# Kernel tuning notes

Measured on AMD Instinct MI355X. Metric: run time of the kernel, lower is better.

Reference implementation:

```python
import jax, jax.numpy as jnp
import numpy as np

EMBED_DIM = 1024
NUM_HEADS = 16
HEAD_DIM = 64
B, S = 4, 2048


def setup_inputs() -> dict:
    key = jax.random.key(0)
    ks = jax.random.split(key, 5)
    std = 0.02
    x = jax.random.normal(ks[0], (B, S, EMBED_DIM), dtype=jnp.float32)
    Wq = std * jax.random.normal(ks[1], (NUM_HEADS, EMBED_DIM, HEAD_DIM), dtype=jnp.float32)
    Wk = std * jax.random.normal(ks[2], (NUM_HEADS, EMBED_DIM, HEAD_DIM), dtype=jnp.float32)
    Wv = std * jax.random.normal(ks[3], (NUM_HEADS, EMBED_DIM, HEAD_DIM), dtype=jnp.float32)
    Wo = std * jax.random.normal(ks[4], (NUM_HEADS, HEAD_DIM, EMBED_DIM), dtype=jnp.float32)
    bq = jnp.zeros((NUM_HEADS, HEAD_DIM), dtype=jnp.float32)
    bk = jnp.zeros((NUM_HEADS, HEAD_DIM), dtype=jnp.float32)
    bv = jnp.zeros((NUM_HEADS, HEAD_DIM), dtype=jnp.float32)
    bo = jnp.zeros((EMBED_DIM,), dtype=jnp.float32)
    return {"x": x, "Wq": Wq, "bq": bq, "Wk": Wk, "bk": bk,
            "Wv": Wv, "bv": bv, "Wo": Wo, "bo": bo}


def reference(x, Wq, bq, Wk, bk, Wv, bv, Wo, bo):
    # q,k,v: [b, s, n, h]
    q = jnp.einsum('bsd,ndh->bsnh', x, Wq) + bq
    k = jnp.einsum('bsd,ndh->bsnh', x, Wk) + bk
    v = jnp.einsum('bsd,ndh->bsnh', x, Wv) + bv
    scale = 1.0 / (HEAD_DIM ** 0.5)
    # non-causal full attention matrix [b, n, s, t]
    attn = jnp.einsum('bsnh,btnh->bnst', q, k) * scale
    attn = jax.nn.softmax(attn, axis=-1)
    after = jnp.einsum('bnst,btnh->bsnh', attn, v)
    out = jnp.einsum('bsnh,nhd->bsd', after, Wo) + bo
    return out
```

## Files before the change

### kernel.cpp

```cpp
#include <hip/hip_runtime.h>

typedef __bf16 bf16;
typedef bf16 bf16x8 __attribute__((ext_vector_type(8)));
typedef bf16 bf16x4 __attribute__((ext_vector_type(4)));
typedef float f32x4 __attribute__((ext_vector_type(4)));

constexpr int Bb = 4, Ss = 2048, Dd = 1024, NH = 16, HD = 64;
constexpr int BS = Bb * Ss;
constexpr int QKV_LD = 3 * Dd;
constexpr float CSC = 0.18033688011112042f;

__device__ __forceinline__ int sw(int row, int col) {
  return (row << 6) + (col ^ ((row & 7) << 3));
}

__device__ __forceinline__ void g2l16(const bf16* g, bf16* l) {
  __builtin_amdgcn_global_load_lds(
      (const __attribute__((address_space(1))) void*)g,
      (__attribute__((address_space(3))) void*)l, 16, 0, 0);
}

__global__ void convert_x(const float* __restrict__ x, bf16* __restrict__ xb) {
  int o = (blockIdx.x * 256 + threadIdx.x) * 4;
  f32x4 v = *(const f32x4*)&x[o];
  bf16x4 r = {(bf16)v[0], (bf16)v[1], (bf16)v[2], (bf16)v[3]};
  *(bf16x4*)&xb[o] = r;
}

__global__ void prep_weights(const float* __restrict__ Wq, const float* __restrict__ Wk,
                             const float* __restrict__ Wv, const float* __restrict__ Wo,
                             const float* __restrict__ bq, const float* __restrict__ bk,
                             const float* __restrict__ bv,
                             bf16* __restrict__ WT_all, bf16* __restrict__ WoT,
                             float* __restrict__ bias_all) {
  int o = blockIdx.x * 256 + threadIdx.x;
  int sel = blockIdx.y;
  if (sel < 3) {
    const float* W = (sel == 0) ? Wq : (sel == 1) ? Wk : Wv;
    float scale = (sel == 0) ? CSC : 1.0f;
    int nq = o >> 10, d = o & 1023;
    int head = nq >> 6, h = nq & 63;
    WT_all[(sel << 20) + o] = (bf16)(W[head * 65536 + d * 64 + h] * scale);
    if (o < 1024) {
      const float* bb = (sel == 0) ? bq : (sel == 1) ? bk : bv;
      bias_all[sel * 1024 + o] = bb[o] * scale;
    }
  } else {
    int dd = o >> 10, c = o & 1023;
    WoT[o] = (bf16)Wo[c * 1024 + dd];
  }
}

template <typename OutT, bool VOUT>
__global__ __launch_bounds__(256) void gemm128(const bf16* __restrict__ A,
                                               const bf16* __restrict__ BT,
                                               const float* __restrict__ bias,
                                               OutT* __restrict__ C, int ldc,
                                               bf16* __restrict__ VTout) {
  __shared__ __align__(16) bf16 As[128 * 64];
  __shared__ __align__(16) bf16 Bs[128 * 64];
  const int t = threadIdx.x;
  const int w = t >> 6, l = t & 63, q = l >> 4, lm = l & 15;
  const int wm = w & 1, wn = w >> 1;
  const int m0 = blockIdx.x * 128, n0 = blockIdx.y * 128;
  constexpr int K = 1024;
  int ro[4], co[4];
#pragma unroll
  for (int i = 0; i < 4; ++i) {
    int o = i * 256 + t;
    ro[i] = o >> 3;
    co[i] = ((o & 7) ^ ((o >> 3) & 7)) << 3;
  }
  const int lbase = (t & 192) * 8;
  f32x4 acc[4][4] = {};
  for (int k0 = 0; k0 < K; k0 += 64) {
    __syncthreads();
#pragma unroll
    for (int i = 0; i < 4; ++i)
      g2l16(&A[(size_t)(m0 + ro[i]) * K + k0 + co[i]], &As[i * 2048 + lbase]);
#pragma unroll
    for (int i = 0; i < 4; ++i)
      g2l16(&BT[(size_t)(n0 + ro[i]) * K + k0 + co[i]], &Bs[i * 2048 + lbase]);
    __syncthreads();
#pragma unroll
    for (int kh = 0; kh < 2; ++kh) {
      bf16x8 a[4], b[4];
#pragma unroll
      for (int i = 0; i < 4; ++i)
        a[i] = *(const bf16x8*)&As[sw(wm * 64 + i * 16 + lm, kh * 32 + q * 8)];
#pragma unroll
      for (int i = 0; i < 4; ++i)
        b[i] = *(const bf16x8*)&Bs[sw(wn * 64 + i * 16 + lm, kh * 32 + q * 8)];
#pragma unroll
      for (int mt = 0; mt < 4; ++mt)
#pragma unroll
        for (int nt = 0; nt < 4; ++nt)
          acc[mt][nt] = __builtin_amdgcn_mfma_f32_16x16x32_bf16(a[mt], b[nt], acc[mt][nt], 0, 0, 0);
    }
  }
  if (VOUT && n0 >= 2048) {
#pragma unroll
    for (int nt = 0; nt < 4; ++nt) {
      int colg = n0 + wn * 64 + nt * 16 + lm;
      float bb = bias[colg];
      int bnh = colg - 2048;
      size_t vbase = (size_t)(bnh >> 6) * 131072 + (size_t)(bnh & 63) * 2048;
#pragma unroll
      for (int mt = 0; mt < 4; ++mt) {
        int row = m0 + wm * 64 + mt * 16 + q * 4;
#pragma unroll
        for (int r = 0; r < 4; ++r) {
          int m = row + r;
          VTout[(size_t)((m >> 11) << 4) * 131072 + vbase + (m & 2047)] =
              (bf16)(acc[mt][nt][r] + bb);
        }
      }
    }
  } else {
#pragma unroll
    for (int nt = 0; nt < 4; ++nt) {
      int col = n0 + wn * 64 + nt * 16 + lm;
      float bb = bias[col];
#pragma unroll
      for (int mt = 0; mt < 4; ++mt) {
        int row = m0 + wm * 64 + mt * 16 + q * 4;
#pragma unroll
        for (int r = 0; r < 4; ++r)
          C[(size_t)(row + r) * ldc + col] = (OutT)(acc[mt][nt][r] + bb);
      }
    }
  }
}

__global__ __launch_bounds__(256) void attn(const bf16* __restrict__ QKV,
                                            const bf16* __restrict__ VT,
                                            bf16* __restrict__ after) {
  __shared__ __align__(16) bf16 QPs[128 * 64];
  __shared__ __align__(16) bf16 Ks[2][64 * 64];
  __shared__ __align__(16) bf16 Vs[2][64 * 64];
  const int t = threadIdx.x;
  const int w = t >> 6, l = t & 63, q = l >> 4, lm = l & 15;
  const int s0 = blockIdx.x * 128;
  const int bn = blockIdx.y, b = bn >> 4, n = bn & 15;
  const bf16* Qb = QKV + (size_t)(b * 2048) * QKV_LD + n * 64;
  const bf16* Kb = Qb + 1024;
  const bf16* Vtb = VT + (size_t)bn * 64 * 2048;
  int ro[4], co[4];
#pragma unroll
  for (int i = 0; i < 4; ++i) {
    int o = i * 256 + t;
    ro[i] = o >> 3;
    co[i] = ((o & 7) ^ ((o >> 3) & 7)) << 3;
  }
  const int lbase = (t & 192) * 8;
#pragma unroll
  for (int i = 0; i < 4; ++i)
    g2l16(&Qb[(size_t)(s0 + ro[i]) * QKV_LD + co[i]], &QPs[i * 2048 + lbase]);
  __syncthreads();
  bf16x8 qa[2][2];
#pragma unroll
  for (int mt = 0; mt < 2; ++mt)
#pragma unroll
    for (int kh = 0; kh < 2; ++kh)
      qa[mt][kh] = *(const bf16x8*)&QPs[sw(w * 32 + mt * 16 + lm, kh * 32 + q * 8)];

  f32x4 o_acc[2][4] = {};
  float rs[2] = {0.f, 0.f};
  for (int t0 = 0; t0 < Ss; t0 += 128) {
    __syncthreads();
#pragma unroll
    for (int j = 0; j < 2; ++j)
#pragma unroll
      for (int i = 0; i < 2; ++i) {
        g2l16(&Kb[(size_t)(t0 + j * 64 + ro[i]) * QKV_LD + co[i]], &Ks[j][i * 2048 + lbase]);
        g2l16(&Vtb[(size_t)ro[i] * 2048 + t0 + j * 64 + co[i]], &Vs[j][i * 2048 + lbase]);
      }
    __syncthreads();
#pragma unroll
    for (int j = 0; j < 2; ++j) {
      f32x4 sc[2][4] = {};
#pragma unroll
      for (int kh = 0; kh < 2; ++kh) {
        bf16x8 kb[4];
#pragma unroll
        for (int c = 0; c < 4; ++c)
          kb[c] = *(const bf16x8*)&Ks[j][sw(c * 16 + lm, kh * 32 + q * 8)];
#pragma unroll
        for (int mt = 0; mt < 2; ++mt)
#pragma unroll
          for (int c = 0; c < 4; ++c)
            sc[mt][c] = __builtin_amdgcn_mfma_f32_16x16x32_bf16(kb[c], qa[mt][kh], sc[mt][c], 0, 0, 0);
      }
#pragma unroll
      for (int mt = 0; mt < 2; ++mt) {
        int s = w * 32 + mt * 16 + lm;
#pragma unroll
        for (int c = 0; c < 4; ++c) {
          bf16x4 pk;
#pragma unroll
          for (int r = 0; r < 4; ++r) {
            float p = __builtin_amdgcn_exp2f(sc[mt][c][r]);
            rs[mt] += p;
            pk[r] = (bf16)p;
          }
          *(bf16x4*)&QPs[(s << 6) + ((((c << 2) + q) ^ lm) << 2)] = pk;
        }
      }
#pragma unroll
      for (int kh = 0; kh < 2; ++kh) {
        bf16x8 pa[2], vb[4];
#pragma unroll
        for (int mt = 0; mt < 2; ++mt) {
          int s = w * 32 + mt * 16 + lm;
          bf16x4 lo = *(const bf16x4*)&QPs[(s << 6) + ((((kh << 3) + (q << 1)) ^ lm) << 2)];
          bf16x4 hi = *(const bf16x4*)&QPs[(s << 6) + ((((kh << 3) + (q << 1) + 1) ^ lm) << 2)];
          pa[mt] = __builtin_shufflevector(lo, hi, 0, 1, 2, 3, 4, 5, 6, 7);
        }
#pragma unroll
        for (int c = 0; c < 4; ++c)
          vb[c] = *(const bf16x8*)&Vs[j][sw(c * 16 + lm, kh * 32 + q * 8)];
#pragma unroll
        for (int mt = 0; mt < 2; ++mt)
#pragma unroll
          for (int c = 0; c < 4; ++c)
            o_acc[mt][c] = __builtin_amdgcn_mfma_f32_16x16x32_bf16(pa[mt], vb[c], o_acc[mt][c], 0, 0, 0);
      }
    }
  }
#pragma unroll
  for (int mt = 0; mt < 2; ++mt) {
    float v = rs[mt];
    v += __shfl_xor(v, 16);
    v += __shfl_xor(v, 32);
    rs[mt] = v;
  }
#pragma unroll
  for (int mt = 0; mt < 2; ++mt)
#pragma unroll
    for (int r = 0; r < 4; ++r) {
      float inv = 1.f / __shfl(rs[mt], q * 4 + r);
      int srow = s0 + w * 32 + mt * 16 + q * 4 + r;
      size_t base = (size_t)(b * 2048 + srow) * 1024 + n * 64;
#pragma unroll
      for (int c = 0; c < 4; ++c)
        after[base + c * 16 + lm] = (bf16)(o_acc[mt][c][r] * inv);
    }
}

extern "C" void kernel_launch(void* const* d_in, const int* in_sizes, int n_in,
                              void* d_out, int out_size, void* d_ws, size_t ws_size,
                              hipStream_t stream) {
  const float* x  = (const float*)d_in[0];
  const float* Wq = (const float*)d_in[1];
  const float* bq = (const float*)d_in[2];
  const float* Wk = (const float*)d_in[3];
  const float* bk = (const float*)d_in[4];
  const float* Wv = (const float*)d_in[5];
  const float* bv = (const float*)d_in[6];
  const float* Wo = (const float*)d_in[7];
  const float* bo = (const float*)d_in[8];
  float* out = (float*)d_out;

  bf16* WT_all    = (bf16*)d_ws;
  bf16* WoT       = WT_all + (size_t)3072 * 1024;
  float* bias_all = (float*)(WoT + (size_t)1024 * 1024);
  bf16* xb        = (bf16*)(bias_all + 4096);
  bf16* QKVb      = xb + (size_t)BS * Dd;
  bf16* VTb       = QKVb + (size_t)BS * QKV_LD;
  bf16* after     = VTb + (size_t)Bb * NH * HD * Ss;

  convert_x<<<dim3(BS * Dd / 1024), dim3(256), 0, stream>>>(x, xb);
  prep_weights<<<dim3(4096, 4), dim3(256), 0, stream>>>(Wq, Wk, Wv, Wo, bq, bk, bv,
                                                        WT_all, WoT, bias_all);
  gemm128<bf16, true><<<dim3(BS / 128, 24), dim3(256), 0, stream>>>(xb, WT_all, bias_all,
                                                                    QKVb, QKV_LD, VTb);
  attn<<<dim3(Ss / 128, Bb * NH), dim3(256), 0, stream>>>(QKVb, VTb, after);
  gemm128<float, false><<<dim3(BS / 128, 8), dim3(256), 0, stream>>>(after, WoT, bo,
                                                                     out, 1024, nullptr);
}
```

Before: 300.9 us.

## Tile weight transposes, split V projection into transposed GEMM, double-buffer attention loads

Weight preparation now transposes through shared-memory tiles with vectorized loads and stores instead of strided scalar gathers. The V projection runs as a separate GEMM with swapped operands, so the transposed V layout is written directly. The attention kernel now software-pipelines K/V tiles: the next 64-key tile is prefetched into a double buffer while the current one is computed, and it uses one barrier per iteration. Row sums are computed with an MFMA against a ones vector instead of scalar adds and shuffles, the P buffer gets a padded layout, occupancy is hinted at 3 blocks, and blocks are remapped for L2 locality. This adds one kernel launch and makes the synchronization more intricate.

```diff
diff --git a/kernel.cpp b/kernel.cpp
--- a/kernel.cpp
+++ b/kernel.cpp
@@ -7,7 +7,6 @@
 
 constexpr int Bb = 4, Ss = 2048, Dd = 1024, NH = 16, HD = 64;
 constexpr int BS = Bb * Ss;
-constexpr int QKV_LD = 3 * Dd;
 constexpr float CSC = 0.18033688011112042f;
 
 __device__ __forceinline__ int sw(int row, int col) {
@@ -27,41 +26,74 @@
   *(bf16x4*)&xb[o] = r;
 }
 
-__global__ void prep_weights(const float* __restrict__ Wq, const float* __restrict__ Wk,
-                             const float* __restrict__ Wv, const float* __restrict__ Wo,
-                             const float* __restrict__ bq, const float* __restrict__ bk,
-                             const float* __restrict__ bv,
-                             bf16* __restrict__ WT_all, bf16* __restrict__ WoT,
-                             float* __restrict__ bias_all) {
-  int o = blockIdx.x * 256 + threadIdx.x;
-  int sel = blockIdx.y;
+__global__ void prep(const float* __restrict__ Wq, const float* __restrict__ Wk,
+                     const float* __restrict__ Wv, const float* __restrict__ Wo,
+                     const float* __restrict__ bq, const float* __restrict__ bk,
+                     const float* __restrict__ bv,
+                     bf16* __restrict__ WT_all, bf16* __restrict__ WoT,
+                     float* __restrict__ bias_all) {
+  __shared__ bf16 Ts[64 * 72];
+  const int t = threadIdx.x;
+  const int sel = blockIdx.y;
   if (sel < 3) {
     const float* W = (sel == 0) ? Wq : (sel == 1) ? Wk : Wv;
     float scale = (sel == 0) ? CSC : 1.0f;
-    int nq = o >> 10, d = o & 1023;
-    int head = nq >> 6, h = nq & 63;
-    WT_all[(sel << 20) + o] = (bf16)(W[head * 65536 + d * 64 + h] * scale);
-    if (o < 1024) {
-      const float* bb = (sel == 0) ? bq : (sel == 1) ? bk : bv;
-      bias_all[sel * 1024 + o] = bb[o] * scale;
-    }
-  } else {
-    int dd = o >> 10, c = o & 1023;
-    WoT[o] = (bf16)Wo[c * 1024 + dd];
-  }
-}
-
-template <typename OutT, bool VOUT>
+    int head = blockIdx.x >> 4, dt = blockIdx.x & 15;
+    const float* src = W + head * 65536 + dt * 64 * 64;
+#pragma unroll
+    for (int i = 0; i < 4; ++i) {
+      int idx = i * 256 + t;
+      int dr = idx >> 4, hc = (idx & 15) * 4;
+      f32x4 v = *(const f32x4*)&src[dr * 64 + hc];
+#pragma unroll
+      for (int k = 0; k < 4; ++k) Ts[(hc + k) * 72 + dr] = (bf16)(v[k] * scale);
+    }
+    __syncthreads();
+    bf16* dst = WT_all + (size_t)sel * 1048576 + (size_t)(head * 64) * 1024 + dt * 64;
+#pragma unroll
+    for (int i = 0; i < 2; ++i) {
+      int idx = i * 256 + t;
+      int hr = idx >> 3, ch = (idx & 7) * 8;
+      *(bf16x8*)&dst[(size_t)hr * 1024 + ch] = *(const bf16x8*)&Ts[hr * 72 + ch];
+    }
+  } else if (sel == 3) {
+    int ct = blockIdx.x >> 4, dt = blockIdx.x & 15;
+    const float* src = Wo + (size_t)(ct * 64) * 1024 + dt * 64;
+#pragma unroll
+    for (int i = 0; i < 4; ++i) {
+      int idx = i * 256 + t;
+      int cr = idx >> 4, dc = (idx & 15) * 4;
+      f32x4 v = *(const f32x4*)&src[(size_t)cr * 1024 + dc];
+#pragma unroll
+      for (int k = 0; k < 4; ++k) Ts[(dc + k) * 72 + cr] = (bf16)v[k];
+    }
+    __syncthreads();
+    bf16* dst = WoT + (size_t)(dt * 64) * 1024 + ct * 64;
+#pragma unroll
+    for (int i = 0; i < 2; ++i) {
+      int idx = i * 256 + t;
+      int dr = idx >> 3, ch = (idx & 7) * 8;
+      *(bf16x8*)&dst[(size_t)dr * 1024 + ch] = *(const bf16x8*)&Ts[dr * 72 + ch];
+    }
+  } else if (blockIdx.x == 0) {
+    for (int j = t; j < 3072; j += 256) {
+      int s2 = j >> 10;
+      const float* bb = (s2 == 0) ? bq : (s2 == 1) ? bk : bv;
+      bias_all[j] = bb[j & 1023] * (s2 == 0 ? CSC : 1.0f);
+    }
+  }
+}
+
+template <int EPI>
 __global__ __launch_bounds__(256) void gemm128(const bf16* __restrict__ A,
                                                const bf16* __restrict__ BT,
                                                const float* __restrict__ bias,
-                                               OutT* __restrict__ C, int ldc,
-                                               bf16* __restrict__ VTout) {
+                                               void* __restrict__ Cv, int ldc) {
   __shared__ __align__(16) bf16 As[128 * 64];
   __shared__ __align__(16) bf16 Bs[128 * 64];
   const int t = threadIdx.x;
-  const int w = t >> 6, l = t & 63, q = l >> 4, lm = l & 15;
-  const int wm = w & 1, wn = w >> 1;
+  const int l = t & 63, q = l >> 4, lm = l & 15;
+  const int w = t >> 6, wm = w & 1, wn = w >> 1;
   const int m0 = blockIdx.x * 128, n0 = blockIdx.y * 128;
   constexpr int K = 1024;
   int ro[4], co[4];
@@ -98,23 +130,20 @@
           acc[mt][nt] = __builtin_amdgcn_mfma_f32_16x16x32_bf16(a[mt], b[nt], acc[mt][nt], 0, 0, 0);
     }
   }
-  if (VOUT && n0 >= 2048) {
+  if (EPI == 1) {
+    bf16* VT = (bf16*)Cv;
 #pragma unroll
     for (int nt = 0; nt < 4; ++nt) {
-      int colg = n0 + wn * 64 + nt * 16 + lm;
-      float bb = bias[colg];
-      int bnh = colg - 2048;
-      size_t vbase = (size_t)(bnh >> 6) * 131072 + (size_t)(bnh & 63) * 2048;
-#pragma unroll
-      for (int mt = 0; mt < 4; ++mt) {
-        int row = m0 + wm * 64 + mt * 16 + q * 4;
+      int sg = n0 + wn * 64 + nt * 16 + lm;
+      size_t sb = (size_t)(sg >> 11) * 2097152 + (sg & 2047);
+#pragma unroll
+      for (int mt = 0; mt < 4; ++mt)
 #pragma unroll
         for (int r = 0; r < 4; ++r) {
-          int m = row + r;
-          VTout[(size_t)((m >> 11) << 4) * 131072 + vbase + (m & 2047)] =
-              (bf16)(acc[mt][nt][r] + bb);
+          int m = m0 + wm * 64 + mt * 16 + q * 4 + r;
+          VT[sb + (size_t)(m >> 6) * 131072 + (size_t)(m & 63) * 2048] =
+              (bf16)(acc[mt][nt][r] + bias[m]);
         }
-      }
     }
   } else {
 #pragma unroll
@@ -125,26 +154,32 @@
       for (int mt = 0; mt < 4; ++mt) {
         int row = m0 + wm * 64 + mt * 16 + q * 4;
 #pragma unroll
-        for (int r = 0; r < 4; ++r)
-          C[(size_t)(row + r) * ldc + col] = (OutT)(acc[mt][nt][r] + bb);
+        for (int r = 0; r < 4; ++r) {
+          if (EPI == 2)
+            ((float*)Cv)[(size_t)(row + r) * ldc + col] = acc[mt][nt][r] + bb;
+          else
+            ((bf16*)Cv)[(size_t)(row + r) * ldc + col] = (bf16)(acc[mt][nt][r] + bb);
+        }
       }
     }
   }
 }
 
-__global__ __launch_bounds__(256) void attn(const bf16* __restrict__ QKV,
-                                            const bf16* __restrict__ VT,
-                                            bf16* __restrict__ after) {
-  __shared__ __align__(16) bf16 QPs[128 * 64];
+__global__ __launch_bounds__(256, 3) void attn(const bf16* __restrict__ QK,
+                                               const bf16* __restrict__ VT,
+                                               bf16* __restrict__ after) {
   __shared__ __align__(16) bf16 Ks[2][64 * 64];
   __shared__ __align__(16) bf16 Vs[2][64 * 64];
+  __shared__ __align__(16) bf16 Ps[128 * 72];
   const int t = threadIdx.x;
-  const int w = t >> 6, l = t & 63, q = l >> 4, lm = l & 15;
-  const int s0 = blockIdx.x * 128;
-  const int bn = blockIdx.y, b = bn >> 4, n = bn & 15;
-  const bf16* Qb = QKV + (size_t)(b * 2048) * QKV_LD + n * 64;
+  const int l = t & 63, q = l >> 4, lm = l & 15, w = t >> 6;
+  const int f = blockIdx.x;
+  const int bn = (f & 7) | ((f >> 7) << 3);
+  const int s0 = ((f >> 3) & 15) * 128;
+  const int b = bn >> 4, n = bn & 15;
+  const bf16* Qb = QK + (size_t)(b * 2048) * 2048 + n * 64;
   const bf16* Kb = Qb + 1024;
-  const bf16* Vtb = VT + (size_t)bn * 64 * 2048;
+  const bf16* Vtb = VT + (size_t)bn * 131072;
   int ro[4], co[4];
 #pragma unroll
   for (int i = 0; i < 4; ++i) {
@@ -153,92 +188,87 @@
     co[i] = ((o & 7) ^ ((o >> 3) & 7)) << 3;
   }
   const int lbase = (t & 192) * 8;
+  bf16* Kflat = &Ks[0][0];
 #pragma unroll
   for (int i = 0; i < 4; ++i)
-    g2l16(&Qb[(size_t)(s0 + ro[i]) * QKV_LD + co[i]], &QPs[i * 2048 + lbase]);
+    g2l16(&Qb[(size_t)(s0 + ro[i]) * 2048 + co[i]], Kflat + i * 2048 + lbase);
   __syncthreads();
   bf16x8 qa[2][2];
 #pragma unroll
   for (int mt = 0; mt < 2; ++mt)
 #pragma unroll
     for (int kh = 0; kh < 2; ++kh)
-      qa[mt][kh] = *(const bf16x8*)&QPs[sw(w * 32 + mt * 16 + lm, kh * 32 + q * 8)];
-
+      qa[mt][kh] = *(const bf16x8*)&Kflat[sw(w * 32 + mt * 16 + lm, kh * 32 + q * 8)];
+  __syncthreads();
+#pragma unroll
+  for (int i = 0; i < 2; ++i) {
+    g2l16(&Kb[(size_t)ro[i] * 2048 + co[i]], &Ks[0][i * 2048 + lbase]);
+    g2l16(&Vtb[(size_t)ro[i] * 2048 + co[i]], &Vs[0][i * 2048 + lbase]);
+  }
   f32x4 o_acc[2][4] = {};
-  float rs[2] = {0.f, 0.f};
-  for (int t0 = 0; t0 < Ss; t0 += 128) {
-    __syncthreads();
-#pragma unroll
-    for (int j = 0; j < 2; ++j)
+  f32x4 rsum[2] = {};
+  const bf16x8 ones = {(bf16)1.f, (bf16)1.f, (bf16)1.f, (bf16)1.f,
+                       (bf16)1.f, (bf16)1.f, (bf16)1.f, (bf16)1.f};
+  for (int rd = 0; rd < 32; ++rd) {
+    const int cur = rd & 1;
+    __syncthreads();
+    if (rd < 31) {
+      int t0n = (rd + 1) * 64, nb = cur ^ 1;
 #pragma unroll
       for (int i = 0; i < 2; ++i) {
-        g2l16(&Kb[(size_t)(t0 + j * 64 + ro[i]) * QKV_LD + co[i]], &Ks[j][i * 2048 + lbase]);
-        g2l16(&Vtb[(size_t)ro[i] * 2048 + t0 + j * 64 + co[i]], &Vs[j][i * 2048 + lbase]);
+        g2l16(&Kb[(size_t)(t0n + ro[i]) * 2048 + co[i]], &Ks[nb][i * 2048 + lbase]);
+        g2l16(&Vtb[(size_t)ro[i] * 2048 + t0n + co[i]], &Vs[nb][i * 2048 + lbase]);
       }
-    __syncthreads();
-#pragma unroll
-    for (int j = 0; j < 2; ++j) {
-      f32x4 sc[2][4] = {};
-#pragma unroll
-      for (int kh = 0; kh < 2; ++kh) {
-        bf16x8 kb[4];
+    }
+    f32x4 sc[2][4] = {};
+#pragma unroll
+    for (int kh = 0; kh < 2; ++kh) {
+      bf16x8 kb[4];
+#pragma unroll
+      for (int c = 0; c < 4; ++c)
+        kb[c] = *(const bf16x8*)&Ks[cur][sw(c * 16 + lm, kh * 32 + q * 8)];
+#pragma unroll
+      for (int mt = 0; mt < 2; ++mt)
 #pragma unroll
         for (int c = 0; c < 4; ++c)
-          kb[c] = *(const bf16x8*)&Ks[j][sw(c * 16 + lm, kh * 32 + q * 8)];
-#pragma unroll
-        for (int mt = 0; mt < 2; ++mt)
-#pragma unroll
-          for (int c = 0; c < 4; ++c)
-            sc[mt][c] = __builtin_amdgcn_mfma_f32_16x16x32_bf16(kb[c], qa[mt][kh], sc[mt][c], 0, 0, 0);
+          sc[mt][c] = __builtin_amdgcn_mfma_f32_16x16x32_bf16(kb[c], qa[mt][kh], sc[mt][c], 0, 0, 0);
+    }
+#pragma unroll
+    for (int mt = 0; mt < 2; ++mt) {
+      int srow = w * 32 + mt * 16 + lm;
+#pragma unroll
+      for (int c = 0; c < 4; ++c) {
+        bf16x4 pk;
+#pragma unroll
+        for (int r = 0; r < 4; ++r)
+          pk[r] = (bf16)__builtin_amdgcn_exp2f(sc[mt][c][r]);
+        *(bf16x4*)&Ps[srow * 72 + (c * 4 + q) * 4] = pk;
       }
-#pragma unroll
-      for (int mt = 0; mt < 2; ++mt) {
-        int s = w * 32 + mt * 16 + lm;
-#pragma unroll
-        for (int c = 0; c < 4; ++c) {
-          bf16x4 pk;
-#pragma unroll
-          for (int r = 0; r < 4; ++r) {
-            float p = __builtin_amdgcn_exp2f(sc[mt][c][r]);
-            rs[mt] += p;
-            pk[r] = (bf16)p;
-          }
-          *(bf16x4*)&QPs[(s << 6) + ((((c << 2) + q) ^ lm) << 2)] = pk;
-        }
-      }
-#pragma unroll
-      for (int kh = 0; kh < 2; ++kh) {
-        bf16x8 pa[2], vb[4];
-#pragma unroll
-        for (int mt = 0; mt < 2; ++mt) {
-          int s = w * 32 + mt * 16 + lm;
-          bf16x4 lo = *(const bf16x4*)&QPs[(s << 6) + ((((kh << 3) + (q << 1)) ^ lm) << 2)];
-          bf16x4 hi = *(const bf16x4*)&QPs[(s << 6) + ((((kh << 3) + (q << 1) + 1) ^ lm) << 2)];
-          pa[mt] = __builtin_shufflevector(lo, hi, 0, 1, 2, 3, 4, 5, 6, 7);
-        }
+    }
+#pragma unroll
+    for (int kh = 0; kh < 2; ++kh) {
+      bf16x8 pa[2], vb[4];
+#pragma unroll
+      for (int mt = 0; mt < 2; ++mt)
+        pa[mt] = *(const bf16x8*)&Ps[(w * 32 + mt * 16 + lm) * 72 + (kh * 8 + q * 2) * 4];
+#pragma unroll
+      for (int c = 0; c < 4; ++c)
+        vb[c] = *(const bf16x8*)&Vs[cur][sw(c * 16 + lm, kh * 32 + q * 8)];
+#pragma unroll
+      for (int mt = 0; mt < 2; ++mt)
+        rsum[mt] = __builtin_amdgcn_mfma_f32_16x16x32_bf16(pa[mt], ones, rsum[mt], 0, 0, 0);
+#pragma unroll
+      for (int mt = 0; mt < 2; ++mt)
 #pragma unroll
         for (int c = 0; c < 4; ++c)
-          vb[c] = *(const bf16x8*)&Vs[j][sw(c * 16 + lm, kh * 32 + q * 8)];
-#pragma unroll
-        for (int mt = 0; mt < 2; ++mt)
-#pragma unroll
-          for (int c = 0; c < 4; ++c)
-            o_acc[mt][c] = __builtin_amdgcn_mfma_f32_16x16x32_bf16(pa[mt], vb[c], o_acc[mt][c], 0, 0, 0);
-      }
-    }
-  }
-#pragma unroll
-  for (int mt = 0; mt < 2; ++mt) {
-    float v = rs[mt];
-    v += __shfl_xor(v, 16);
-    v += __shfl_xor(v, 32);
-    rs[mt] = v;
+          o_acc[mt][c] = __builtin_amdgcn_mfma_f32_16x16x32_bf16(pa[mt], vb[c], o_acc[mt][c], 0, 0, 0);
+    }
   }
 #pragma unroll
   for (int mt = 0; mt < 2; ++mt)
 #pragma unroll
     for (int r = 0; r < 4; ++r) {
-      float inv = 1.f / __shfl(rs[mt], q * 4 + r);
+      float inv = 1.f / rsum[mt][r];
       int srow = s0 + w * 32 + mt * 16 + q * 4 + r;
       size_t base = (size_t)(b * 2048 + srow) * 1024 + n * 64;
 #pragma unroll
@@ -265,16 +295,16 @@
   bf16* WoT       = WT_all + (size_t)3072 * 1024;
   float* bias_all = (float*)(WoT + (size_t)1024 * 1024);
   bf16* xb        = (bf16*)(bias_all + 4096);
-  bf16* QKVb      = xb + (size_t)BS * Dd;
-  bf16* VTb       = QKVb + (size_t)BS * QKV_LD;
+  bf16* QKb       = xb + (size_t)BS * Dd;
+  bf16* VTb       = QKb + (size_t)BS * 2048;
   bf16* after     = VTb + (size_t)Bb * NH * HD * Ss;
 
   convert_x<<<dim3(BS * Dd / 1024), dim3(256), 0, stream>>>(x, xb);
-  prep_weights<<<dim3(4096, 4), dim3(256), 0, stream>>>(Wq, Wk, Wv, Wo, bq, bk, bv,
-                                                        WT_all, WoT, bias_all);
-  gemm128<bf16, true><<<dim3(BS / 128, 24), dim3(256), 0, stream>>>(xb, WT_all, bias_all,
-                                                                    QKVb, QKV_LD, VTb);
-  attn<<<dim3(Ss / 128, Bb * NH), dim3(256), 0, stream>>>(QKVb, VTb, after);
-  gemm128<float, false><<<dim3(BS / 128, 8), dim3(256), 0, stream>>>(after, WoT, bo,
-                                                                     out, 1024, nullptr);
-}
+  prep<<<dim3(256, 5), dim3(256), 0, stream>>>(Wq, Wk, Wv, Wo, bq, bk, bv,
+                                               WT_all, WoT, bias_all);
+  gemm128<0><<<dim3(64, 16), dim3(256), 0, stream>>>(xb, WT_all, bias_all, QKb, 2048);
+  gemm128<1><<<dim3(8, 64), dim3(256), 0, stream>>>(WT_all + (size_t)2048 * 1024, xb,
+                                                    bias_all + 2048, VTb, 0);
+  attn<<<dim3(1024), dim3(256), 0, stream>>>(QKb, VTb, after);
+  gemm128<2><<<dim3(64, 8), dim3(256), 0, stream>>>(after, WoT, bo, out, 1024);
+}
```

Result: faster. 290.5 us (-3.5%).
